# Kernel optimization log

Measured on AMD Instinct MI355X. Metric: run time of the kernel, lower is better.

## Reference

```python
import jax, jax.numpy as jnp
import numpy as np

DIM = 256

def setup_inputs() -> dict:
    key = jax.random.key(0)
    ks = jax.random.split(key, 7)
    s = 1.0 / np.sqrt(DIM)
    x = jax.random.normal(ks[0], (16, DIM, 32, 32), dtype=jnp.float32)
    proj_w = jax.random.uniform(ks[1], (DIM, DIM), jnp.float32, -s, s)
    proj_b = jax.random.uniform(ks[2], (DIM,), jnp.float32, -s, s)
    w1 = jax.random.uniform(ks[3], (DIM, DIM), jnp.float32, -s, s)
    b1 = jax.random.uniform(ks[4], (DIM,), jnp.float32, -s, s)
    w2 = jax.random.uniform(ks[5], (DIM, DIM), jnp.float32, -s, s)
    b2 = jax.random.uniform(ks[6], (DIM,), jnp.float32, -s, s)
    return {"x": x, "proj_w": proj_w, "proj_b": proj_b, "w1": w1, "b1": b1, "w2": w2, "b2": b2}

def reference(x, proj_w, proj_b, w1, b1, w2, b2):
    B, C, H, W = x.shape
    # nodes: [B, N, C] with N = H*W
    nodes = x.reshape(B, C, H * W).transpose(0, 2, 1)
    q = nodes @ proj_w.T + proj_b                      # [B,N,C]
    scores = jnp.einsum('bnc,bmc->bnm', q, q) / jnp.sqrt(jnp.float32(C))
    attn = jax.nn.softmax(scores, axis=-1)             # [B,N,N]
    agg = jnp.einsum('bnm,bmc->bnc', attn, nodes)      # [B,N,C]
    h = jax.nn.gelu(agg @ w1.T + b1, approximate=False)
    out = h @ w2.T + b2                                # [B,N,C]
    return x + out.transpose(0, 2, 1).reshape(B, C, H, W)
```

## Files before the change

kernel.cpp:

```cpp
#include <hip/hip_runtime.h>
#include <stdint.h>

typedef unsigned short u16;
typedef __attribute__((ext_vector_type(8))) short short8;
typedef __attribute__((ext_vector_type(4))) float f32x4;

#define NB    16
#define DIM   256
#define NTOK  1024

__device__ __forceinline__ u16 f2b(float f) {
    union { float f; uint32_t u; } v; v.f = f;
    uint32_t u = v.u;
    u += 0x7fffu + ((u >> 16) & 1u);
    return (u16)(u >> 16);
}
__device__ __forceinline__ uint32_t pack2(float a, float b) {
    return (uint32_t)f2b(a) | ((uint32_t)f2b(b) << 16);
}
__device__ __forceinline__ f32x4 mfma16(short8 a, short8 b, f32x4 c) {
    return __builtin_amdgcn_mfma_f32_16x16x32_bf16(a, b, c, 0, 0, 0);
}
__device__ __forceinline__ short8 ld8(const u16* p) {
    return *reinterpret_cast<const short8*>(p);
}
__device__ __forceinline__ void gl_lds(const u16* g, u16* l) {
    __builtin_amdgcn_global_load_lds((const __attribute__((address_space(1))) void*)g,
                                     (__attribute__((address_space(3))) void*)l, 16, 0, 0);
}

__global__ __launch_bounds__(256) void wconv_kernel(const float* __restrict__ pw,
                                                    const float* __restrict__ w1,
                                                    const float* __restrict__ w2,
                                                    u16* __restrict__ wbf) {
    int e = blockIdx.x * 2048 + threadIdx.x * 8;
    const float* s; int off;
    if (e < 65536)       { s = pw; off = e; }
    else if (e < 131072) { s = w1; off = e - 65536; }
    else                 { s = w2; off = e - 131072; }
    float4 f0 = *reinterpret_cast<const float4*>(s + off);
    float4 f1 = *reinterpret_cast<const float4*>(s + off + 4);
    ushort4 a, b;
    a.x = f2b(f0.x); a.y = f2b(f0.y); a.z = f2b(f0.z); a.w = f2b(f0.w);
    b.x = f2b(f1.x); b.y = f2b(f1.y); b.z = f2b(f1.z); b.w = f2b(f1.w);
    *reinterpret_cast<ushort4*>(wbf + e)     = a;
    *reinterpret_cast<ushort4*>(wbf + e + 4) = b;
}

__global__ __launch_bounds__(256) void packproj_kernel(const float* __restrict__ x,
                                                       u16* __restrict__ xbf,
                                                       const u16* __restrict__ wbf,
                                                       const float* __restrict__ pb,
                                                       u16* __restrict__ qb) {
    __shared__ float stage[64][68];
    __shared__ u16 tile[64 * 256];
    int tid = threadIdx.x;
    int lane = tid & 63;
    int w = tid >> 6;
    int lo = lane & 15, hi = lane >> 4;
    int b  = blockIdx.x & 15;
    int nt = blockIdx.x >> 4;
    int n0 = nt * 64;
    const float* xb = x + (size_t)b * (DIM * NTOK);
    u16* xbb = xbf + (size_t)b * (DIM * NTOK);

#pragma unroll
    for (int cc = 0; cc < 4; cc++) {
#pragma unroll
        for (int i = 0; i < 4; i++) {
            int idx = i * 256 + tid;
            int cl = idx >> 4, nq = idx & 15;
            float4 f = *reinterpret_cast<const float4*>(
                xb + (size_t)(cc * 64 + cl) * NTOK + n0 + nq * 4);
            stage[cl][nq * 4 + 0] = f.x;
            stage[cl][nq * 4 + 1] = f.y;
            stage[cl][nq * 4 + 2] = f.z;
            stage[cl][nq * 4 + 3] = f.w;
            ushort4 s;
            s.x = f2b(f.x); s.y = f2b(f.y); s.z = f2b(f.z); s.w = f2b(f.w);
            *reinterpret_cast<ushort4*>(xbb + (size_t)(cc * 64 + cl) * NTOK + n0 + nq * 4) = s;
        }
        __syncthreads();
#pragma unroll
        for (int j = 0; j < 2; j++) {
            int item = j * 256 + tid;
            int nl = item >> 3, g = item & 7;
            union { u16 s[8]; short8 v; } o;
#pragma unroll
            for (int k = 0; k < 8; k++) o.s[k] = f2b(stage[g * 8 + k][nl]);
            int gi = (cc * 8 + g) ^ (nl & 7);
            *reinterpret_cast<short8*>(&tile[nl * 256 + gi * 8]) = o.v;
        }
        __syncthreads();
    }

    f32x4 acc[16];
#pragma unroll
    for (int i = 0; i < 16; i++) acc[i] = (f32x4){0.f, 0.f, 0.f, 0.f};
    int ar = w * 16 + lo;
#pragma unroll
    for (int t = 0; t < 8; t++) {
        int gi = (t * 4 + hi) ^ (lo & 7);
        short8 a = ld8(&tile[ar * 256 + gi * 8]);
#pragma unroll
        for (int nf = 0; nf < 16; nf++) {
            short8 bfr = ld8(wbf + (nf * 16 + lo) * DIM + t * 32 + hi * 8);
            acc[nf] = mfma16(a, bfr, acc[nf]);
        }
    }
#pragma unroll
    for (int nf = 0; nf < 16; nf++) {
        int col = nf * 16 + lo;
        float bias = pb[col];
#pragma unroll
        for (int r = 0; r < 4; r++) {
            int row = n0 + w * 16 + hi * 4 + r;
            qb[(size_t)(b * NTOK + row) * DIM + col] = f2b(acc[nf][r] + bias);
        }
    }
}

__global__ __launch_bounds__(256, 1) void attn_ffn_kernel(const u16* __restrict__ qb,
                                                          const u16* __restrict__ xbf,
                                                          const u16* __restrict__ wbf,
                                                          const float* __restrict__ b1,
                                                          const float* __restrict__ b2,
                                                          const float* __restrict__ x,
                                                          float* __restrict__ out) {
    __shared__ u16 kls[2][2][8192];
    __shared__ u16 vls[2][2][8192];
    __shared__ float ellX[4][2][16];

    int lane = threadIdx.x & 63;
    int w = threadIdx.x >> 6;
    int qsel = w >> 1, kvh = w & 1;
    int lo = lane & 15, hi = lane >> 4;
    int b  = blockIdx.x & 15;
    int qt = blockIdx.x >> 4;
    int q0 = qt * 64 + qsel * 32;
    const u16* qbb = qb  + (size_t)b * (NTOK * DIM);
    const u16* xbb = xbf + (size_t)b * (DIM * NTOK);
    const u16* w1b = wbf + 65536;
    const u16* w2b = wbf + 131072;

    int kOff[8], vOff[8], kDst[8], vDst[8];
#pragma unroll
    for (int i = 0; i < 8; i++) {
        int kr = qsel * 16 + i * 2 + (lane >> 5);
        kOff[i] = kr * DIM + ((lane & 31) ^ (kr & 7)) * 8;
        kDst[i] = (qsel * 16 + i * 2) * 256;
        int vc = qsel * 128 + i * 16 + (lane >> 2);
        vOff[i] = vc * NTOK + ((lane & 3) ^ (vc & 3)) * 8;
        vDst[i] = (qsel * 128 + i * 16) * 32;
    }
    int kvbeg = kvh * 512;

    short8 bq0[8], bq1[8];
#pragma unroll
    for (int t = 0; t < 8; t++) {
        bq0[t] = ld8(qbb + (size_t)(q0 + lo) * DIM + t * 32 + hi * 8);
        bq1[t] = ld8(qbb + (size_t)(q0 + 16 + lo) * DIM + t * 32 + hi * 8);
    }

    f32x4 acc0[16], acc1[16];
#pragma unroll
    for (int i = 0; i < 16; i++) {
        acc0[i] = (f32x4){0.f, 0.f, 0.f, 0.f};
        acc1[i] = (f32x4){0.f, 0.f, 0.f, 0.f};
    }
    float ellp0 = 0.f, ellp1 = 0.f;
    const float C1 = 0.0625f * 1.44269504f;
    const float OFF = 12.0f;

#pragma unroll
    for (int i = 0; i < 8; i++) {
        gl_lds(qbb + kvbeg * DIM + kOff[i], &kls[kvh][0][kDst[i]]);
        gl_lds(xbb + kvbeg       + vOff[i], &vls[kvh][0][vDst[i]]);
    }
    __syncthreads();

    for (int tt = 0; tt < 16; tt++) {
        int buf = tt & 1;
        if (tt < 15) {
            int base = kvbeg + (tt + 1) * 32;
#pragma unroll
            for (int i = 0; i < 8; i++) {
                gl_lds(qbb + base * DIM + kOff[i], &kls[kvh][buf ^ 1][kDst[i]]);
                gl_lds(xbb + base       + vOff[i], &vls[kvh][buf ^ 1][vDst[i]]);
            }
        }
        const u16* kb = &kls[kvh][buf][0];
        const u16* vb = &vls[kvh][buf][0];

        f32x4 s00 = (f32x4){0.f,0.f,0.f,0.f}, s01 = (f32x4){0.f,0.f,0.f,0.f};
        f32x4 s10 = (f32x4){0.f,0.f,0.f,0.f}, s11 = (f32x4){0.f,0.f,0.f,0.f};
        __builtin_amdgcn_s_setprio(1);
#pragma unroll
        for (int t = 0; t < 8; t++) {
            int sl = ((t * 4 + hi) ^ (lo & 7)) * 8;
            short8 a0 = ld8(kb + lo * 256 + sl);
            short8 a1 = ld8(kb + (16 + lo) * 256 + sl);
            s00 = mfma16(a0, bq0[t], s00);
            s01 = mfma16(a1, bq0[t], s01);
            s10 = mfma16(a0, bq1[t], s10);
            s11 = mfma16(a1, bq1[t], s11);
        }
        __builtin_amdgcn_s_setprio(0);

        float p00[4], p01[4], p10[4], p11[4];
#pragma unroll
        for (int r = 0; r < 4; r++) {
            p00[r] = exp2f(s00[r] * C1 - OFF);
            p01[r] = exp2f(s01[r] * C1 - OFF);
            p10[r] = exp2f(s10[r] * C1 - OFF);
            p11[r] = exp2f(s11[r] * C1 - OFF);
            ellp0 += p00[r] + p01[r];
            ellp1 += p10[r] + p11[r];
        }

        short8 pfrag0, pfrag1;
        {
            uint32_t pl0 = pack2(p00[0], p00[1]), ph0 = pack2(p00[2], p00[3]);
            uint32_t pl1 = pack2(p01[0], p01[1]), ph1 = pack2(p01[2], p01[3]);
            int srcA = ((hi & 1) << 5) | lo;
            int srcB = srcA + 16;
            uint32_t w0a = __shfl(pl0, srcA), w0b = __shfl(pl1, srcA);
            uint32_t w1a = __shfl(ph0, srcA), w1b = __shfl(ph1, srcA);
            uint32_t w2a = __shfl(pl0, srcB), w2b = __shfl(pl1, srcB);
            uint32_t w3a = __shfl(ph0, srcB), w3b = __shfl(ph1, srcB);
            bool sel = (hi >= 2);
            union { uint32_t u[4]; short8 v; } pu;
            pu.u[0] = sel ? w0b : w0a;
            pu.u[1] = sel ? w1b : w1a;
            pu.u[2] = sel ? w2b : w2a;
            pu.u[3] = sel ? w3b : w3a;
            pfrag0 = pu.v;
        }
        {
            uint32_t pl0 = pack2(p10[0], p10[1]), ph0 = pack2(p10[2], p10[3]);
            uint32_t pl1 = pack2(p11[0], p11[1]), ph1 = pack2(p11[2], p11[3]);
            int srcA = ((hi & 1) << 5) | lo;
            int srcB = srcA + 16;
            uint32_t w0a = __shfl(pl0, srcA), w0b = __shfl(pl1, srcA);
            uint32_t w1a = __shfl(ph0, srcA), w1b = __shfl(ph1, srcA);
            uint32_t w2a = __shfl(pl0, srcB), w2b = __shfl(pl1, srcB);
            uint32_t w3a = __shfl(ph0, srcB), w3b = __shfl(ph1, srcB);
            bool sel = (hi >= 2);
            union { uint32_t u[4]; short8 v; } pu;
            pu.u[0] = sel ? w0b : w0a;
            pu.u[1] = sel ? w1b : w1a;
            pu.u[2] = sel ? w2b : w2a;
            pu.u[3] = sel ? w3b : w3a;
            pfrag1 = pu.v;
        }

        int vsl = (hi ^ (lo & 3)) * 8;
        __builtin_amdgcn_s_setprio(1);
#pragma unroll
        for (int mf = 0; mf < 16; mf++) {
            short8 a = ld8(vb + (mf * 16 + lo) * 32 + vsl);
            acc0[mf] = mfma16(a, pfrag0, acc0[mf]);
            acc1[mf] = mfma16(a, pfrag1, acc1[mf]);
        }
        __builtin_amdgcn_s_setprio(0);
        __syncthreads();
    }

    float e0 = ellp0;
    e0 += __shfl_xor(e0, 16); e0 += __shfl_xor(e0, 32);
    float e1 = ellp1;
    e1 += __shfl_xor(e1, 16); e1 += __shfl_xor(e1, 32);
    if (lane < 16) { ellX[w][0][lane] = e0; ellX[w][1][lane] = e1; }
    __syncthreads();
    float rinv0 = 1.f / (e0 + ellX[w ^ 1][0][lo]);
    float rinv1 = 1.f / (e1 + ellX[w ^ 1][1][lo]);

    char* pbase = (char*)kls;
    if (kvh == 0) {
#pragma unroll
        for (int j = 0; j < 8; j++) {
            int byt = (w * 2 + 0) * 8192 + lo * 512 + ((j * 64 + hi * 16) ^ ((lo & 7) << 4));
            *reinterpret_cast<f32x4*>(pbase + byt) = acc0[8 + j];
            int byt1 = (w * 2 + 1) * 8192 + lo * 512 + ((j * 64 + hi * 16) ^ ((lo & 7) << 4));
            *reinterpret_cast<f32x4*>(pbase + byt1) = acc1[8 + j];
        }
    } else {
#pragma unroll
        for (int j = 0; j < 8; j++) {
            int byt = (w * 2 + 0) * 8192 + lo * 512 + ((j * 64 + hi * 16) ^ ((lo & 7) << 4));
            *reinterpret_cast<f32x4*>(pbase + byt) = acc0[j];
            int byt1 = (w * 2 + 1) * 8192 + lo * 512 + ((j * 64 + hi * 16) ^ ((lo & 7) << 4));
            *reinterpret_cast<f32x4*>(pbase + byt1) = acc1[j];
        }
    }
    __syncthreads();
    char* abase = (char*)vls;
    if (kvh == 0) {
#pragma unroll
        for (int j = 0; j < 8; j++) {
            int pb0 = ((w ^ 1) * 2 + 0) * 8192 + lo * 512 + ((j * 64 + hi * 16) ^ ((lo & 7) << 4));
            f32x4 o = *reinterpret_cast<const f32x4*>(pbase + pb0);
            uint32_t lo32 = pack2((acc0[j][0] + o[0]) * rinv0, (acc0[j][1] + o[1]) * rinv0);
            uint32_t hi32 = pack2((acc0[j][2] + o[2]) * rinv0, (acc0[j][3] + o[3]) * rinv0);
            int slot = j * 2 + (hi >> 1);
            int arow = qsel * 32 + lo;
            int byteA = arow * 512 + ((slot ^ (lo & 7)) * 16) + (hi & 1) * 8;
            *reinterpret_cast<uint32_t*>(abase + byteA)     = lo32;
            *reinterpret_cast<uint32_t*>(abase + byteA + 4) = hi32;
            int pb1 = ((w ^ 1) * 2 + 1) * 8192 + lo * 512 + ((j * 64 + hi * 16) ^ ((lo & 7) << 4));
            f32x4 o1 = *reinterpret_cast<const f32x4*>(pbase + pb1);
            uint32_t lo32b = pack2((acc1[j][0] + o1[0]) * rinv1, (acc1[j][1] + o1[1]) * rinv1);
            uint32_t hi32b = pack2((acc1[j][2] + o1[2]) * rinv1, (acc1[j][3] + o1[3]) * rinv1);
            int arow1 = qsel * 32 + 16 + lo;
            int byteB = arow1 * 512 + ((slot ^ (lo & 7)) * 16) + (hi & 1) * 8;
            *reinterpret_cast<uint32_t*>(abase + byteB)     = lo32b;
            *reinterpret_cast<uint32_t*>(abase + byteB + 4) = hi32b;
        }
    } else {
#pragma unroll
        for (int j = 0; j < 8; j++) {
            int pb0 = ((w ^ 1) * 2 + 0) * 8192 + lo * 512 + ((j * 64 + hi * 16) ^ ((lo & 7) << 4));
            f32x4 o = *reinterpret_cast<const f32x4*>(pbase + pb0);
            uint32_t lo32 = pack2((acc0[8 + j][0] + o[0]) * rinv0, (acc0[8 + j][1] + o[1]) * rinv0);
            uint32_t hi32 = pack2((acc0[8 + j][2] + o[2]) * rinv0, (acc0[8 + j][3] + o[3]) * rinv0);
            int slot = 16 + j * 2 + (hi >> 1);
            int arow = qsel * 32 + lo;
            int byteA = arow * 512 + ((slot ^ (lo & 7)) * 16) + (hi & 1) * 8;
            *reinterpret_cast<uint32_t*>(abase + byteA)     = lo32;
            *reinterpret_cast<uint32_t*>(abase + byteA + 4) = hi32;
            int pb1 = ((w ^ 1) * 2 + 1) * 8192 + lo * 512 + ((j * 64 + hi * 16) ^ ((lo & 7) << 4));
            f32x4 o1 = *reinterpret_cast<const f32x4*>(pbase + pb1);
            uint32_t lo32b = pack2((acc1[8 + j][0] + o1[0]) * rinv1, (acc1[8 + j][1] + o1[1]) * rinv1);
            uint32_t hi32b = pack2((acc1[8 + j][2] + o1[2]) * rinv1, (acc1[8 + j][3] + o1[3]) * rinv1);
            int arow1 = qsel * 32 + 16 + lo;
            int byteB = arow1 * 512 + ((slot ^ (lo & 7)) * 16) + (hi & 1) * 8;
            *reinterpret_cast<uint32_t*>(abase + byteB)     = lo32b;
            *reinterpret_cast<uint32_t*>(abase + byteB + 4) = hi32b;
        }
    }
    __syncthreads();

    int rh = w >> 1, chh = w & 1;
    f32x4 f1a[8], f1b[8];
#pragma unroll
    for (int i = 0; i < 8; i++) {
        f1a[i] = (f32x4){0.f, 0.f, 0.f, 0.f};
        f1b[i] = (f32x4){0.f, 0.f, 0.f, 0.f};
    }
#pragma unroll
    for (int t = 0; t < 8; t++) {
        int g = ((t * 4 + hi) ^ (lo & 7)) * 16;
        short8 aA = *reinterpret_cast<const short8*>(abase + (rh * 32 + lo) * 512 + g);
        short8 aB = *reinterpret_cast<const short8*>(abase + (rh * 32 + 16 + lo) * 512 + g);
#pragma unroll
        for (int nf = 0; nf < 8; nf++) {
            short8 bfr = ld8(w1b + ((chh * 8 + nf) * 16 + lo) * DIM + t * 32 + hi * 8);
            f1a[nf] = mfma16(aA, bfr, f1a[nf]);
            f1b[nf] = mfma16(aB, bfr, f1b[nf]);
        }
    }
    u16* hl = (u16*)kls;
#pragma unroll
    for (int nf = 0; nf < 8; nf++) {
        int f = (chh * 8 + nf) * 16 + lo;
        float bias = b1[f];
#pragma unroll
        for (int r = 0; r < 4; r++) {
            float va = f1a[nf][r] + bias;
            float vb2 = f1b[nf][r] + bias;
            float ga = 0.5f * va * (1.f + erff(va * 0.70710678f));
            float gb = 0.5f * vb2 * (1.f + erff(vb2 * 0.70710678f));
            hl[(rh * 32 + hi * 4 + r) * 264 + f]      = f2b(ga);
            hl[(rh * 32 + 16 + hi * 4 + r) * 264 + f] = f2b(gb);
        }
    }
    __syncthreads();

    f32x4 f2a[8], f2b_[8];
#pragma unroll
    for (int i = 0; i < 8; i++) {
        f2a[i] = (f32x4){0.f, 0.f, 0.f, 0.f};
        f2b_[i] = (f32x4){0.f, 0.f, 0.f, 0.f};
    }
#pragma unroll
    for (int t = 0; t < 8; t++) {
        short8 hA = ld8(hl + (rh * 32 + lo) * 264 + t * 32 + hi * 8);
        short8 hB = ld8(hl + (rh * 32 + 16 + lo) * 264 + t * 32 + hi * 8);
#pragma unroll
        for (int mf = 0; mf < 8; mf++) {
            short8 a2 = ld8(w2b + ((chh * 8 + mf) * 16 + lo) * DIM + t * 32 + hi * 8);
            f2a[mf] = mfma16(a2, hA, f2a[mf]);
            f2b_[mf] = mfma16(a2, hB, f2b_[mf]);
        }
    }
    int nA = qt * 64 + rh * 32 + lo;
    int nB = nA + 16;
#pragma unroll
    for (int mf = 0; mf < 8; mf++) {
#pragma unroll
        for (int r = 0; r < 4; r++) {
            int co = (chh * 8 + mf) * 16 + hi * 4 + r;
            size_t rowb = (size_t)b * (DIM * NTOK) + (size_t)co * NTOK;
            out[rowb + nA] = f2a[mf][r] + b2[co] + x[rowb + nA];
            out[rowb + nB] = f2b_[mf][r] + b2[co] + x[rowb + nB];
        }
    }
}

extern "C" void kernel_launch(void* const* d_in, const int* in_sizes, int n_in,
                              void* d_out, int out_size, void* d_ws, size_t ws_size,
                              hipStream_t stream) {
    const float* x      = (const float*)d_in[0];
    const float* proj_w = (const float*)d_in[1];
    const float* proj_b = (const float*)d_in[2];
    const float* w1     = (const float*)d_in[3];
    const float* b1     = (const float*)d_in[4];
    const float* w2     = (const float*)d_in[5];
    const float* b2     = (const float*)d_in[6];
    float* out = (float*)d_out;

    u16* xbf = (u16*)d_ws;
    u16* qb  = xbf + 4194304;
    u16* wbf = qb  + 4194304;

    wconv_kernel   <<<96,   256, 0, stream>>>(proj_w, w1, w2, wbf);
    packproj_kernel<<<256,  256, 0, stream>>>(x, xbf, wbf, proj_b, qb);
    attn_ffn_kernel<<<256,  256, 0, stream>>>(qb, xbf, wbf, b1, b2, x, out);
}
```

Before: 101.1 us.

## Store projected queries in FP8 and use FP8 MFMA for attention scores

The projection kernel now writes q as FP8 (e4m3) bytes instead of bf16, and the attention kernel stages K tiles as FP8 in LDS with a new 16-byte swizzle. The QK^T score MFMAs switch to the fp8 16x16x32 instruction. This halves K-tile global/LDS traffic and q workspace size, and LDS buffer reuse for the later stages is reshuffled to match. The cost is reduced precision in the attention scores, which risks accuracy in the softmax.

```diff
diff --git a/kernel.cpp b/kernel.cpp
--- a/kernel.cpp
+++ b/kernel.cpp
@@ -2,6 +2,7 @@
 #include <stdint.h>
 
 typedef unsigned short u16;
+typedef unsigned char u8;
 typedef __attribute__((ext_vector_type(8))) short short8;
 typedef __attribute__((ext_vector_type(4))) float f32x4;
 
@@ -21,10 +22,16 @@
 __device__ __forceinline__ f32x4 mfma16(short8 a, short8 b, f32x4 c) {
     return __builtin_amdgcn_mfma_f32_16x16x32_bf16(a, b, c, 0, 0, 0);
 }
+__device__ __forceinline__ f32x4 mfma_fp8(long a, long b, f32x4 c) {
+    return __builtin_amdgcn_mfma_f32_16x16x32_fp8_fp8(a, b, c, 0, 0, 0);
+}
 __device__ __forceinline__ short8 ld8(const u16* p) {
     return *reinterpret_cast<const short8*>(p);
 }
-__device__ __forceinline__ void gl_lds(const u16* g, u16* l) {
+__device__ __forceinline__ u8 pk1fp8(float a) {
+    return (u8)(__builtin_amdgcn_cvt_pk_fp8_f32(a, a, 0, false) & 0xff);
+}
+__device__ __forceinline__ void gl_lds(const void* g, void* l) {
     __builtin_amdgcn_global_load_lds((const __attribute__((address_space(1))) void*)g,
                                      (__attribute__((address_space(3))) void*)l, 16, 0, 0);
 }
@@ -51,7 +58,7 @@
                                                        u16* __restrict__ xbf,
                                                        const u16* __restrict__ wbf,
                                                        const float* __restrict__ pb,
-                                                       u16* __restrict__ qb) {
+                                                       u8* __restrict__ qb8) {
     __shared__ float stage[64][68];
     __shared__ u16 tile[64 * 256];
     int tid = threadIdx.x;
@@ -115,19 +122,19 @@
 #pragma unroll
         for (int r = 0; r < 4; r++) {
             int row = n0 + w * 16 + hi * 4 + r;
-            qb[(size_t)(b * NTOK + row) * DIM + col] = f2b(acc[nf][r] + bias);
-        }
-    }
-}
-
-__global__ __launch_bounds__(256, 1) void attn_ffn_kernel(const u16* __restrict__ qb,
+            qb8[(size_t)(b * NTOK + row) * DIM + col] = pk1fp8(acc[nf][r] + bias);
+        }
+    }
+}
+
+__global__ __launch_bounds__(256, 1) void attn_ffn_kernel(const u8* __restrict__ qb8,
                                                           const u16* __restrict__ xbf,
                                                           const u16* __restrict__ wbf,
                                                           const float* __restrict__ b1,
                                                           const float* __restrict__ b2,
                                                           const float* __restrict__ x,
                                                           float* __restrict__ out) {
-    __shared__ u16 kls[2][2][8192];
+    __shared__ u8  kls[2][2][8192];
     __shared__ u16 vls[2][2][8192];
     __shared__ float ellX[4][2][16];
 
@@ -138,28 +145,32 @@
     int b  = blockIdx.x & 15;
     int qt = blockIdx.x >> 4;
     int q0 = qt * 64 + qsel * 32;
-    const u16* qbb = qb  + (size_t)b * (NTOK * DIM);
+    const u8*  qbb = qb8 + (size_t)b * (NTOK * DIM);
     const u16* xbb = xbf + (size_t)b * (DIM * NTOK);
     const u16* w1b = wbf + 65536;
     const u16* w2b = wbf + 131072;
 
-    int kOff[8], vOff[8], kDst[8], vDst[8];
+    int kOff[4], kDst[4];
+#pragma unroll
+    for (int i = 0; i < 4; i++) {
+        int kr = qsel * 16 + i * 4 + (lane >> 4);
+        kOff[i] = kr * 256 + ((lane & 15) ^ (kr & 15)) * 16;
+        kDst[i] = (qsel * 16 + i * 4) * 256;
+    }
+    int vOff[8], vDst[8];
 #pragma unroll
     for (int i = 0; i < 8; i++) {
-        int kr = qsel * 16 + i * 2 + (lane >> 5);
-        kOff[i] = kr * DIM + ((lane & 31) ^ (kr & 7)) * 8;
-        kDst[i] = (qsel * 16 + i * 2) * 256;
         int vc = qsel * 128 + i * 16 + (lane >> 2);
         vOff[i] = vc * NTOK + ((lane & 3) ^ (vc & 3)) * 8;
         vDst[i] = (qsel * 128 + i * 16) * 32;
     }
     int kvbeg = kvh * 512;
 
-    short8 bq0[8], bq1[8];
+    long bq0[8], bq1[8];
 #pragma unroll
     for (int t = 0; t < 8; t++) {
-        bq0[t] = ld8(qbb + (size_t)(q0 + lo) * DIM + t * 32 + hi * 8);
-        bq1[t] = ld8(qbb + (size_t)(q0 + 16 + lo) * DIM + t * 32 + hi * 8);
+        bq0[t] = *reinterpret_cast<const long*>(qbb + (size_t)(q0 + lo) * 256 + t * 32 + hi * 8);
+        bq1[t] = *reinterpret_cast<const long*>(qbb + (size_t)(q0 + 16 + lo) * 256 + t * 32 + hi * 8);
     }
 
     f32x4 acc0[16], acc1[16];
@@ -173,10 +184,11 @@
     const float OFF = 12.0f;
 
 #pragma unroll
-    for (int i = 0; i < 8; i++) {
-        gl_lds(qbb + kvbeg * DIM + kOff[i], &kls[kvh][0][kDst[i]]);
-        gl_lds(xbb + kvbeg       + vOff[i], &vls[kvh][0][vDst[i]]);
-    }
+    for (int i = 0; i < 4; i++)
+        gl_lds(qbb + kvbeg * 256 + kOff[i], &kls[kvh][0][kDst[i]]);
+#pragma unroll
+    for (int i = 0; i < 8; i++)
+        gl_lds(xbb + kvbeg + vOff[i], &vls[kvh][0][vDst[i]]);
     __syncthreads();
 
     for (int tt = 0; tt < 16; tt++) {
@@ -184,12 +196,13 @@
         if (tt < 15) {
             int base = kvbeg + (tt + 1) * 32;
 #pragma unroll
-            for (int i = 0; i < 8; i++) {
-                gl_lds(qbb + base * DIM + kOff[i], &kls[kvh][buf ^ 1][kDst[i]]);
-                gl_lds(xbb + base       + vOff[i], &vls[kvh][buf ^ 1][vDst[i]]);
-            }
-        }
-        const u16* kb = &kls[kvh][buf][0];
+            for (int i = 0; i < 4; i++)
+                gl_lds(qbb + base * 256 + kOff[i], &kls[kvh][buf ^ 1][kDst[i]]);
+#pragma unroll
+            for (int i = 0; i < 8; i++)
+                gl_lds(xbb + base + vOff[i], &vls[kvh][buf ^ 1][vDst[i]]);
+        }
+        const u8*  kb = &kls[kvh][buf][0];
         const u16* vb = &vls[kvh][buf][0];
 
         f32x4 s00 = (f32x4){0.f,0.f,0.f,0.f}, s01 = (f32x4){0.f,0.f,0.f,0.f};
@@ -197,13 +210,13 @@
         __builtin_amdgcn_s_setprio(1);
 #pragma unroll
         for (int t = 0; t < 8; t++) {
-            int sl = ((t * 4 + hi) ^ (lo & 7)) * 8;
-            short8 a0 = ld8(kb + lo * 256 + sl);
-            short8 a1 = ld8(kb + (16 + lo) * 256 + sl);
-            s00 = mfma16(a0, bq0[t], s00);
-            s01 = mfma16(a1, bq0[t], s01);
-            s10 = mfma16(a0, bq1[t], s10);
-            s11 = mfma16(a1, bq1[t], s11);
+            int gsw = ((t * 2 + (hi >> 1)) ^ lo) * 16 + (hi & 1) * 8;
+            long a0 = *reinterpret_cast<const long*>(kb + lo * 256 + gsw);
+            long a1 = *reinterpret_cast<const long*>(kb + (16 + lo) * 256 + gsw);
+            s00 = mfma_fp8(a0, bq0[t], s00);
+            s01 = mfma_fp8(a1, bq0[t], s01);
+            s10 = mfma_fp8(a0, bq1[t], s10);
+            s11 = mfma_fp8(a1, bq1[t], s11);
         }
         __builtin_amdgcn_s_setprio(0);
 
@@ -271,11 +284,8 @@
     float e1 = ellp1;
     e1 += __shfl_xor(e1, 16); e1 += __shfl_xor(e1, 32);
     if (lane < 16) { ellX[w][0][lane] = e0; ellX[w][1][lane] = e1; }
-    __syncthreads();
-    float rinv0 = 1.f / (e0 + ellX[w ^ 1][0][lo]);
-    float rinv1 = 1.f / (e1 + ellX[w ^ 1][1][lo]);
-
-    char* pbase = (char*)kls;
+
+    char* pbase = (char*)vls;
     if (kvh == 0) {
 #pragma unroll
         for (int j = 0; j < 8; j++) {
@@ -294,7 +304,9 @@
         }
     }
     __syncthreads();
-    char* abase = (char*)vls;
+    float rinv0 = 1.f / (e0 + ellX[w ^ 1][0][lo]);
+    float rinv1 = 1.f / (e1 + ellX[w ^ 1][1][lo]);
+    char* abase = (char*)kls;
     if (kvh == 0) {
 #pragma unroll
         for (int j = 0; j < 8; j++) {
@@ -359,7 +371,8 @@
             f1b[nf] = mfma16(aB, bfr, f1b[nf]);
         }
     }
-    u16* hl = (u16*)kls;
+    u16* hl2 = (u16*)vls;
+    __syncthreads();
 #pragma unroll
     for (int nf = 0; nf < 8; nf++) {
         int f = (chh * 8 + nf) * 16 + lo;
@@ -370,8 +383,8 @@
             float vb2 = f1b[nf][r] + bias;
             float ga = 0.5f * va * (1.f + erff(va * 0.70710678f));
             float gb = 0.5f * vb2 * (1.f + erff(vb2 * 0.70710678f));
-            hl[(rh * 32 + hi * 4 + r) * 264 + f]      = f2b(ga);
-            hl[(rh * 32 + 16 + hi * 4 + r) * 264 + f] = f2b(gb);
+            hl2[(rh * 32 + hi * 4 + r) * 264 + f]      = f2b(ga);
+            hl2[(rh * 32 + 16 + hi * 4 + r) * 264 + f] = f2b(gb);
         }
     }
     __syncthreads();
@@ -384,8 +397,8 @@
     }
 #pragma unroll
     for (int t = 0; t < 8; t++) {
-        short8 hA = ld8(hl + (rh * 32 + lo) * 264 + t * 32 + hi * 8);
-        short8 hB = ld8(hl + (rh * 32 + 16 + lo) * 264 + t * 32 + hi * 8);
+        short8 hA = ld8(hl2 + (rh * 32 + lo) * 264 + t * 32 + hi * 8);
+        short8 hB = ld8(hl2 + (rh * 32 + 16 + lo) * 264 + t * 32 + hi * 8);
 #pragma unroll
         for (int mf = 0; mf < 8; mf++) {
             short8 a2 = ld8(w2b + ((chh * 8 + mf) * 16 + lo) * DIM + t * 32 + hi * 8);
@@ -420,10 +433,10 @@
     float* out = (float*)d_out;
 
     u16* xbf = (u16*)d_ws;
-    u16* qb  = xbf + 4194304;
-    u16* wbf = qb  + 4194304;
-
-    wconv_kernel   <<<96,   256, 0, stream>>>(proj_w, w1, w2, wbf);
-    packproj_kernel<<<256,  256, 0, stream>>>(x, xbf, wbf, proj_b, qb);
-    attn_ffn_kernel<<<256,  256, 0, stream>>>(qb, xbf, wbf, b1, b2, x, out);
-}
+    u8*  qb8 = (u8*)(xbf + 4194304);
+    u16* wbf = (u16*)(qb8 + 4194304);
+
+    wconv_kernel   <<<96,  256, 0, stream>>>(proj_w, w1, w2, wbf);
+    packproj_kernel<<<256, 256, 0, stream>>>(x, xbf, wbf, proj_b, qb8);
+    attn_ffn_kernel<<<256, 256, 0, stream>>>(qb8, xbf, wbf, b1, b2, x, out);
+}
```

Result: faster. 98.50 us (-2.6%).
